# Performance work log

Hardware: AMD Instinct MI355X
Metric: run time of the kernel (lower is better)

Reference implementation:

```python
import jax, jax.numpy as jnp
import numpy as np

B, NV, FD = 16, 128, 8192
T_TEMP = 0.2      # self.T
MARGIN = 1.0      # nn.TripletMarginLoss default
EPS = 1e-6        # pairwise_distance eps


def _l2norm(x):
    # torch F.normalize(dim=1): x / max(||x||, 1e-12)
    nrm = jnp.maximum(jnp.linalg.norm(x, axis=-1, keepdims=True), 1e-12)
    return x / nrm


def _ssl_parts(qb, kb, nb, num_gt):
    # qb,kb,nb: [NV, FD] flattened reid embeddings for one image
    qv = _l2norm(qb)[:num_gt]          # [g, FD]
    kv = _l2norm(kb)[:num_gt]          # [g, FD]
    nv = _l2norm(nb)                   # [NV, FD] (negatives are NOT sliced)
    g = num_gt
    S = qv @ kv.T                      # [g, g] all pairwise dots (replaces torch.dot loops)
    # similarity-matrix loss
    sm = jnp.sum((S - jnp.eye(g, dtype=S.dtype)) ** 2) / (g * g)
    # pairwise distances with torch eps convention: ||a - b + eps||_2
    # = sqrt(||a||^2 + ||b||^2 - 2 a.b + 2*eps*(sum(a)-sum(b)) + D*eps^2); ||a||=||b||=1
    sq = qv.sum(axis=1)                # [g]
    sk = kv.sum(axis=1)                # [g]
    const = FD * EPS * EPS
    d_qk = jnp.sqrt(jnp.maximum(2.0 - 2.0 * S + 2.0 * EPS * (sq[:, None] - sk[None, :]) + const, 0.0))
    d_kq = jnp.sqrt(jnp.maximum(2.0 - 2.0 * S.T + 2.0 * EPS * (sk[:, None] - sq[None, :]) + const, 0.0))
    off = 1.0 - jnp.eye(g, dtype=S.dtype)
    # triplet: anc=q_i,pos=k_i,neg=k_j  and  anc=k_i,pos=q_i,neg=q_j, j != i
    tri1 = jnp.sum(jax.nn.relu(jnp.diag(d_qk)[:, None] - d_qk + MARGIN) * off)
    tri2 = jnp.sum(jax.nn.relu(jnp.diag(d_kq)[:, None] - d_kq + MARGIN) * off)
    tri_sum = tri1 + tri2
    # cycle consistency: |q_i.k_j - k_i.q_j| = |S[i,j] - S[j,i]|
    cyc = jnp.sum(jnp.abs(S - S.T) * off) / (g * (g - 1))
    # InfoNCE: l_pos = q_i.k_i, l_neg = q @ n.T
    l_pos = jnp.diag(S)[:, None]       # [g, 1]
    l_neg = qv @ nv.T                  # [g, NV]
    logits = jnp.concatenate([l_pos, l_neg], axis=1) / T_TEMP
    ce = jnp.mean(jax.nn.logsumexp(logits, axis=1) - logits[:, 0])  # CE with labels=0
    return sm, tri_sum, cyc, ce / g


def setup_inputs() -> dict:
    key = jax.random.key(0)
    kq, kk, kn = jax.random.split(key, 3)
    q = jax.random.normal(kq, (B, NV, FD), dtype=jnp.float32)
    k = jax.random.normal(kk, (B, NV, FD), dtype=jnp.float32)
    n = jax.random.normal(kn, (B, NV, FD), dtype=jnp.float32)
    return {"q": q, "k": k, "n": n, "num_gt": NV}


def reference(q, k, n, num_gt):
    sm, tri, cyc, ce = jax.vmap(lambda a, b, c: _ssl_parts(a, b, c, num_gt))(q, k, n)
    tri_cnt = 2 * num_gt * (num_gt - 1)
    # original bug: tri_loss accumulates across batches while tri_cnt resets,
    # so each batch contributes cumsum(tri)[b] / tri_cnt
    ssl = jnp.sum(sm) + jnp.sum(jnp.cumsum(tri)) / tri_cnt + jnp.sum(cyc) + jnp.sum(ce)
    return ssl
```

## Files before the change

kernel.cpp:

```cpp
#include <hip/hip_runtime.h>
#include <cstdint>
#include <cstddef>

#define B_N   16
#define G_N   128
#define FD_N  8192
#define KSPLIT 16
#define KC    512
#define BK2   32
#define NITER 16

typedef unsigned short u16;
typedef u16  u16x4 __attribute__((ext_vector_type(4)));
typedef u16  u16x8 __attribute__((ext_vector_type(8)));
typedef __bf16 bf16x8 __attribute__((ext_vector_type(8)));
typedef float f32x16 __attribute__((ext_vector_type(16)));

#define QSUM_P   0
#define QSSQ_P   32768
#define KSUM_P   65536
#define KSSQ_P   98304
#define NSSQ_P   131072
#define SM_ROW   163840
#define CE_ROW   165888
#define S_OFF    167936
#define CONTRIB  430080
#define PART_OFF_F 430208

__device__ __forceinline__ u16 f2bf(float f) {
    uint32_t u = __float_as_uint(f);
    u += 0x7FFFu + ((u >> 16) & 1u);
    return (u16)(u >> 16);
}

#define LDS_BARRIER() asm volatile("s_waitcnt lgkmcnt(0)\n\ts_barrier" ::: "memory")

__global__ __launch_bounds__(512, 4)
void k_gemm(const float* __restrict__ q, const float* __restrict__ kM,
            const float* __restrict__ nM, float* __restrict__ ws)
{
    __shared__ __align__(16) u16 sA[G_N * BK2];
    __shared__ __align__(16) u16 sB[G_N * BK2];

    const int tid = threadIdx.x;
    const int blk = blockIdx.x;
    const int b    = blk >> 5;
    const int rem  = blk & 31;
    const int half = rem >> 4;
    const int kch  = rem & 15;

    const int r0 = tid >> 3;
    const int c8 = tid & 7;

    const size_t mat_off = (size_t)b * (G_N * FD_N) + (size_t)kch * KC + (size_t)(c8 * 4);
    const float* Ap = q + mat_off;
    const float* Bp = (half ? nM : kM) + mat_off;

    float4 la[2][2], lb[2][2];
    float aS[2] = {0,0}, aQ[2] = {0,0}, bS[2] = {0,0}, bQ[2] = {0,0};

    #pragma unroll
    for (int st = 0; st < 2; ++st) {
        const float* A2 = Ap + st * BK2;
        const float* B2 = Bp + st * BK2;
        #pragma unroll
        for (int i = 0; i < 2; ++i) {
            la[st][i] = *(const float4*)(A2 + (size_t)(r0 + 64*i) * FD_N);
            lb[st][i] = *(const float4*)(B2 + (size_t)(r0 + 64*i) * FD_N);
        }
    }

    const int lane  = tid & 63;
    const int wv    = tid >> 6;
    const int wm    = wv >> 2;
    const int wn    = wv & 3;
    const int khalf = lane >> 5;
    const int lrow  = lane & 31;
    const int rA0 = wm*64 + lrow;
    const int rB0 = wn*32 + lrow;

    f32x16 acc[2];
    #pragma unroll
    for (int mb = 0; mb < 2; ++mb)
      #pragma unroll
      for (int e = 0; e < 16; ++e) acc[mb][e] = 0.f;

    for (int kb = 0; kb < NITER; ++kb) {
        const int st = kb & 1;
        LDS_BARRIER();
        #pragma unroll
        for (int i = 0; i < 2; ++i) {
            int row = r0 + 64*i;
            int wof = row*BK2 + (((c8>>1) ^ (row&3))<<3) + ((c8&1)<<2);
            float4 v = la[st][i];
            aS[i] += v.x + v.y + v.z + v.w;
            aQ[i] += v.x*v.x + v.y*v.y + v.z*v.z + v.w*v.w;
            u16x4 h; h[0]=f2bf(v.x); h[1]=f2bf(v.y); h[2]=f2bf(v.z); h[3]=f2bf(v.w);
            *(u16x4*)(sA + wof) = h;
            v = lb[st][i];
            bS[i] += v.x + v.y + v.z + v.w;
            bQ[i] += v.x*v.x + v.y*v.y + v.z*v.z + v.w*v.w;
            u16x4 h2; h2[0]=f2bf(v.x); h2[1]=f2bf(v.y); h2[2]=f2bf(v.z); h2[3]=f2bf(v.w);
            *(u16x4*)(sB + wof) = h2;
        }
        LDS_BARRIER();
        if (kb + 2 < NITER) {
            const float* A2 = Ap + (kb+2) * BK2;
            const float* B2 = Bp + (kb+2) * BK2;
            #pragma unroll
            for (int i = 0; i < 2; ++i) {
                la[st][i] = *(const float4*)(A2 + (size_t)(r0 + 64*i) * FD_N);
                lb[st][i] = *(const float4*)(B2 + (size_t)(r0 + 64*i) * FD_N);
            }
        }
        #pragma unroll
        for (int s = 0; s < 2; ++s) {
            int chunk = s*2 + khalf;
            bf16x8 af[2], bfv;
            #pragma unroll
            for (int mb = 0; mb < 2; ++mb) {
                int row = rA0 + mb*32;
                u16x8 raw = *(const u16x8*)(sA + row*BK2 + ((chunk ^ (row&3))<<3));
                af[mb] = __builtin_bit_cast(bf16x8, raw);
            }
            u16x8 rawb = *(const u16x8*)(sB + rB0*BK2 + ((chunk ^ (rB0&3))<<3));
            bfv = __builtin_bit_cast(bf16x8, rawb);
            acc[0] = __builtin_amdgcn_mfma_f32_32x32x16_bf16(af[0], bfv, acc[0], 0, 0, 0);
            acc[1] = __builtin_amdgcn_mfma_f32_32x32x16_bf16(af[1], bfv, acc[1], 0, 0, 0);
        }
    }

    u16* part = (u16*)(ws + PART_OFF_F) + ((size_t)blk << 14);
    #pragma unroll
    for (int mb = 0; mb < 2; ++mb) {
        int col = wn*32 + lrow;
        int rbase = wm*64 + mb*32 + 4*khalf;
        #pragma unroll
        for (int reg = 0; reg < 16; ++reg) {
            int row = rbase + (reg & 3) + 8*(reg >> 2);
            part[row*G_N + col] = f2bf(acc[mb][reg]);
        }
    }

    #pragma unroll
    for (int i = 0; i < 2; ++i) {
        float sa = aS[i], qa = aQ[i], sb = bS[i], qb = bQ[i];
        #pragma unroll
        for (int m = 4; m >= 1; m >>= 1) {
            sa += __shfl_xor(sa, m, 64); qa += __shfl_xor(qa, m, 64);
            sb += __shfl_xor(sb, m, 64); qb += __shfl_xor(qb, m, 64);
        }
        if (c8 == 0) {
            int o = kch*2048 + b*G_N + (r0 + 64*i);
            if (half == 0) {
                ws[QSUM_P + o] = sa; ws[QSSQ_P + o] = qa;
                ws[KSUM_P + o] = sb; ws[KSSQ_P + o] = qb;
            } else {
                ws[NSSQ_P + o] = qb;
            }
        }
    }
}

__global__ __launch_bounds__(256)
void k_red2(float* __restrict__ ws)
{
    const int blk  = blockIdx.x;
    const int b    = blk >> 4;
    const int half = (blk >> 3) & 1;
    const int rg   = blk & 7;
    const int t    = threadIdx.x;
    const int lr   = t >> 4;
    const int i    = rg*16 + lr;
    const int c8   = t & 15;
    __shared__ float nrm[128];
    __shared__ float invq_s[16];

    if (t < 128) {
        float ss = 0.f;
        const float* p = ws + (half ? NSSQ_P : KSSQ_P) + b*G_N + t;
        #pragma unroll
        for (int kc2 = 0; kc2 < KSPLIT; ++kc2) ss += p[kc2*2048];
        nrm[t] = 1.f / fmaxf(sqrtf(ss), 1e-12f);
    } else if (t < 144) {
        float ss = 0.f;
        const float* p = ws + QSSQ_P + b*G_N + rg*16 + (t - 128);
        #pragma unroll
        for (int kc2 = 0; kc2 < KSPLIT; ++kc2) ss += p[kc2*2048];
        invq_s[t-128] = 1.f / fmaxf(sqrtf(ss), 1e-12f);
    }
    __syncthreads();

    const u16* part = (const u16*)(ws + PART_OFF_F);
    float s[8] = {0,0,0,0,0,0,0,0};
    #pragma unroll
    for (int kc2 = 0; kc2 < KSPLIT; ++kc2) {
        size_t idx = ((size_t)(b*32 + half*16 + kc2) << 14) + i*G_N + c8*8;
        u16x8 h = *(const u16x8*)(part + idx);
        #pragma unroll
        for (int e = 0; e < 8; ++e)
            s[e] += __uint_as_float(((uint32_t)h[e]) << 16);
    }
    const float iq = invq_s[lr];
    if (half == 0) {
        float smacc = 0.f;
        float S8[8];
        #pragma unroll
        for (int e = 0; e < 8; ++e) {
            int j = c8*8 + e;
            S8[e] = s[e] * iq * nrm[j];
            float d = S8[e] - (j == i ? 1.f : 0.f);
            smacc += d*d;
        }
        float* Sp = ws + S_OFF + (size_t)b*16384 + i*G_N + c8*8;
        float4 w0 = {S8[0],S8[1],S8[2],S8[3]};
        float4 w1 = {S8[4],S8[5],S8[6],S8[7]};
        *(float4*)Sp = w0; *(float4*)(Sp+4) = w1;
        #pragma unroll
        for (int m = 8; m >= 1; m >>= 1) smacc += __shfl_xor(smacc, m, 64);
        if (c8 == 0) ws[SM_ROW + b*G_N + i] = smacc;
    } else {
        float eacc = 0.f;
        #pragma unroll
        for (int e = 0; e < 8; ++e)
            eacc += __expf(5.f * s[e] * iq * nrm[c8*8+e]);
        #pragma unroll
        for (int m = 8; m >= 1; m >>= 1) eacc += __shfl_xor(eacc, m, 64);
        if (c8 == 0) ws[CE_ROW + b*G_N + i] = eacc;
    }
}

__global__ __launch_bounds__(256)
void k_epi(float* __restrict__ ws)
{
    const int blk = blockIdx.x;
    const int b   = blk >> 3;
    const int i0  = (blk & 7) * 16;
    const int t   = threadIdx.x;
    __shared__ float sqv[128], skv[128], ddq[128], ddk[128];
    __shared__ float rbuf[4];
    const float c0 = (float)FD_N * 1e-6f * 1e-6f;

    const float* S = ws + S_OFF + (size_t)b * 16384;
    if (t < 128) {
        float qs=0, qq=0, ks=0, kq=0;
        #pragma unroll
        for (int kc2 = 0; kc2 < KSPLIT; ++kc2) {
            int o = kc2*2048 + b*G_N + t;
            qs += ws[QSUM_P + o]; qq += ws[QSSQ_P + o];
            ks += ws[KSUM_P + o]; kq += ws[KSSQ_P + o];
        }
        float iq = 1.f/fmaxf(sqrtf(qq),1e-12f);
        float ik = 1.f/fmaxf(sqrtf(kq),1e-12f);
        float sq = qs*iq, sk = ks*ik;
        sqv[t]=sq; skv[t]=sk;
        float Stt = S[t*G_N + t];
        ddq[t] = sqrtf(fmaxf(2.f - 2.f*Stt + 2e-6f*(sq-sk) + c0, 0.f));
        ddk[t] = sqrtf(fmaxf(2.f - 2.f*Stt + 2e-6f*(sk-sq) + c0, 0.f));
    }
    __syncthreads();

    float tri=0.f, cyc=0.f, ce=0.f, sm=0.f;
    #pragma unroll
    for (int p = 0; p < 8; ++p) {
        int idx = p*256 + t;
        int i = i0 + (idx >> 7), j = idx & 127;
        if (i != j) {
            float S_ij = S[i*G_N + j];
            float dqk = sqrtf(fmaxf(2.f - 2.f*S_ij + 2e-6f*(sqv[i]-skv[j]) + c0, 0.f));
            tri += fmaxf(ddq[i] - dqk + 1.f, 0.f);
            float dkq = sqrtf(fmaxf(2.f - 2.f*S_ij + 2e-6f*(skv[j]-sqv[i]) + c0, 0.f));
            tri += fmaxf(ddk[j] - dkq + 1.f, 0.f);
            cyc += fabsf(S_ij - S[j*G_N + i]);
        }
    }
    if (t < 16) {
        int r = i0 + t;
        float lp = 5.f * S[r*G_N + r];
        ce = __logf(ws[CE_ROW + b*G_N + r] + __expf(lp)) - lp;
        sm = ws[SM_ROW + b*G_N + r];
    }
    float contrib = sm * (1.f/16384.f) + cyc * (1.f/16256.f) + ce * (1.f/16384.f)
                  + (float)(B_N - b) * tri * (1.f/32512.f);
    #pragma unroll
    for (int m = 32; m >= 1; m >>= 1) contrib += __shfl_xor(contrib, m, 64);
    if ((t & 63) == 0) rbuf[t >> 6] = contrib;
    __syncthreads();
    if (t == 0) ws[CONTRIB + blk] = rbuf[0] + rbuf[1] + rbuf[2] + rbuf[3];
}

__global__ void k_fin(const float* __restrict__ ws, float* __restrict__ out)
{
    __shared__ float r2[2];
    int t = threadIdx.x;
    float v = ws[CONTRIB + t];
    #pragma unroll
    for (int m = 32; m >= 1; m >>= 1) v += __shfl_xor(v, m, 64);
    if ((t & 63) == 0) r2[t >> 6] = v;
    __syncthreads();
    if (t == 0) out[0] = r2[0] + r2[1];
}

extern "C" void kernel_launch(void* const* d_in, const int* in_sizes, int n_in,
                              void* d_out, int out_size, void* d_ws, size_t ws_size,
                              hipStream_t stream)
{
    const float* q  = (const float*)d_in[0];
    const float* kM = (const float*)d_in[1];
    const float* nM = (const float*)d_in[2];
    float* ws  = (float*)d_ws;
    float* out = (float*)d_out;

    k_gemm<<<B_N * 2 * KSPLIT, 512, 0, stream>>>(q, kM, nM, ws);
    k_red2<<<256, 256, 0, stream>>>(ws);
    k_epi<<<128, 256, 0, stream>>>(ws);
    k_fin<<<1, 128, 0, stream>>>(ws, out);
}
```

Baseline: 268.6 us.

## Unroll GEMM k-loop by two, change LDS swizzle, fold final reduction into atomics

The GEMM main loop is unrolled by two with named register stages, so the double-buffered prefetch registers are indexed statically instead of through a dynamic stage index. The LDS XOR swizzle now uses (row>>1)&3, which changes the bank-conflict pattern of the bf16 writes and MFMA fragment reads. The final k_fin kernel is removed: k_red2 zeroes the output and k_epi blocks atomically add their contributions, saving one launch. The atomics make the summation order nondeterministic, and correctness relies on k_red2 finishing before k_epi on the same stream.

```diff
diff --git a/kernel.cpp b/kernel.cpp
--- a/kernel.cpp
+++ b/kernel.cpp
@@ -24,8 +24,7 @@
 #define SM_ROW   163840
 #define CE_ROW   165888
 #define S_OFF    167936
-#define CONTRIB  430080
-#define PART_OFF_F 430208
+#define PART_OFF_F 430080
 
 __device__ __forceinline__ u16 f2bf(float f) {
     uint32_t u = __float_as_uint(f);
@@ -56,18 +55,20 @@
     const float* Ap = q + mat_off;
     const float* Bp = (half ? nM : kM) + mat_off;
 
-    float4 la[2][2], lb[2][2];
+    float4 a0[2], b0[2], a1[2], b1[2];
     float aS[2] = {0,0}, aQ[2] = {0,0}, bS[2] = {0,0}, bQ[2] = {0,0};
 
     #pragma unroll
-    for (int st = 0; st < 2; ++st) {
-        const float* A2 = Ap + st * BK2;
-        const float* B2 = Bp + st * BK2;
-        #pragma unroll
-        for (int i = 0; i < 2; ++i) {
-            la[st][i] = *(const float4*)(A2 + (size_t)(r0 + 64*i) * FD_N);
-            lb[st][i] = *(const float4*)(B2 + (size_t)(r0 + 64*i) * FD_N);
-        }
+    for (int i = 0; i < 2; ++i) {
+        size_t ro = (size_t)(r0 + 64*i) * FD_N;
+        a0[i] = *(const float4*)(Ap + ro);
+        b0[i] = *(const float4*)(Bp + ro);
+    }
+    #pragma unroll
+    for (int i = 0; i < 2; ++i) {
+        size_t ro = (size_t)(r0 + 64*i) * FD_N + BK2;
+        a1[i] = *(const float4*)(Ap + ro);
+        b1[i] = *(const float4*)(Bp + ro);
     }
 
     const int lane  = tid & 63;
@@ -79,55 +80,77 @@
     const int rA0 = wm*64 + lrow;
     const int rB0 = wn*32 + lrow;
 
+    int wof[2];
+    #pragma unroll
+    for (int i = 0; i < 2; ++i) {
+        int row = r0 + 64*i;
+        wof[i] = row*BK2 + 8*((c8>>1) ^ ((row>>1)&3)) + 4*(c8&1);
+    }
+
     f32x16 acc[2];
     #pragma unroll
     for (int mb = 0; mb < 2; ++mb)
       #pragma unroll
       for (int e = 0; e < 16; ++e) acc[mb][e] = 0.f;
 
-    for (int kb = 0; kb < NITER; ++kb) {
-        const int st = kb & 1;
+#define STORE_STAGE(AR, BR)                                                   \
+    {                                                                         \
+        _Pragma("unroll")                                                     \
+        for (int i = 0; i < 2; ++i) {                                         \
+            float4 v = AR[i];                                                 \
+            aS[i] += v.x + v.y + v.z + v.w;                                   \
+            aQ[i] += v.x*v.x + v.y*v.y + v.z*v.z + v.w*v.w;                   \
+            u16x4 h; h[0]=f2bf(v.x); h[1]=f2bf(v.y); h[2]=f2bf(v.z); h[3]=f2bf(v.w); \
+            *(u16x4*)(sA + wof[i]) = h;                                       \
+            v = BR[i];                                                        \
+            bS[i] += v.x + v.y + v.z + v.w;                                   \
+            bQ[i] += v.x*v.x + v.y*v.y + v.z*v.z + v.w*v.w;                   \
+            u16x4 h2; h2[0]=f2bf(v.x); h2[1]=f2bf(v.y); h2[2]=f2bf(v.z); h2[3]=f2bf(v.w); \
+            *(u16x4*)(sB + wof[i]) = h2;                                      \
+        }                                                                     \
+    }
+
+#define REFILL(AR, BR, KOFF)                                                  \
+    {                                                                         \
+        _Pragma("unroll")                                                     \
+        for (int i = 0; i < 2; ++i) {                                         \
+            size_t ro = (size_t)(r0 + 64*i) * FD_N + (KOFF);                  \
+            AR[i] = *(const float4*)(Ap + ro);                                \
+            BR[i] = *(const float4*)(Bp + ro);                                \
+        }                                                                     \
+    }
+
+#define MFMA_PHASE()                                                          \
+    {                                                                         \
+        _Pragma("unroll")                                                     \
+        for (int s = 0; s < 2; ++s) {                                         \
+            int chunk = s*2 + khalf;                                          \
+            bf16x8 af0, af1, bfv;                                             \
+            { int row = rA0;                                                  \
+              u16x8 raw = *(const u16x8*)(sA + row*BK2 + 8*(chunk ^ ((row>>1)&3))); \
+              af0 = __builtin_bit_cast(bf16x8, raw); }                        \
+            { int row = rA0 + 32;                                             \
+              u16x8 raw = *(const u16x8*)(sA + row*BK2 + 8*(chunk ^ ((row>>1)&3))); \
+              af1 = __builtin_bit_cast(bf16x8, raw); }                        \
+            { int row = rB0;                                                  \
+              u16x8 raw = *(const u16x8*)(sB + row*BK2 + 8*(chunk ^ ((row>>1)&3))); \
+              bfv = __builtin_bit_cast(bf16x8, raw); }                        \
+            acc[0] = __builtin_amdgcn_mfma_f32_32x32x16_bf16(af0, bfv, acc[0], 0, 0, 0); \
+            acc[1] = __builtin_amdgcn_mfma_f32_32x32x16_bf16(af1, bfv, acc[1], 0, 0, 0); \
+        }                                                                     \
+    }
+
+    for (int kb = 0; kb < NITER; kb += 2) {
         LDS_BARRIER();
-        #pragma unroll
-        for (int i = 0; i < 2; ++i) {
-            int row = r0 + 64*i;
-            int wof = row*BK2 + (((c8>>1) ^ (row&3))<<3) + ((c8&1)<<2);
-            float4 v = la[st][i];
-            aS[i] += v.x + v.y + v.z + v.w;
-            aQ[i] += v.x*v.x + v.y*v.y + v.z*v.z + v.w*v.w;
-            u16x4 h; h[0]=f2bf(v.x); h[1]=f2bf(v.y); h[2]=f2bf(v.z); h[3]=f2bf(v.w);
-            *(u16x4*)(sA + wof) = h;
-            v = lb[st][i];
-            bS[i] += v.x + v.y + v.z + v.w;
-            bQ[i] += v.x*v.x + v.y*v.y + v.z*v.z + v.w*v.w;
-            u16x4 h2; h2[0]=f2bf(v.x); h2[1]=f2bf(v.y); h2[2]=f2bf(v.z); h2[3]=f2bf(v.w);
-            *(u16x4*)(sB + wof) = h2;
-        }
+        STORE_STAGE(a0, b0);
         LDS_BARRIER();
-        if (kb + 2 < NITER) {
-            const float* A2 = Ap + (kb+2) * BK2;
-            const float* B2 = Bp + (kb+2) * BK2;
-            #pragma unroll
-            for (int i = 0; i < 2; ++i) {
-                la[st][i] = *(const float4*)(A2 + (size_t)(r0 + 64*i) * FD_N);
-                lb[st][i] = *(const float4*)(B2 + (size_t)(r0 + 64*i) * FD_N);
-            }
-        }
-        #pragma unroll
-        for (int s = 0; s < 2; ++s) {
-            int chunk = s*2 + khalf;
-            bf16x8 af[2], bfv;
-            #pragma unroll
-            for (int mb = 0; mb < 2; ++mb) {
-                int row = rA0 + mb*32;
-                u16x8 raw = *(const u16x8*)(sA + row*BK2 + ((chunk ^ (row&3))<<3));
-                af[mb] = __builtin_bit_cast(bf16x8, raw);
-            }
-            u16x8 rawb = *(const u16x8*)(sB + rB0*BK2 + ((chunk ^ (rB0&3))<<3));
-            bfv = __builtin_bit_cast(bf16x8, rawb);
-            acc[0] = __builtin_amdgcn_mfma_f32_32x32x16_bf16(af[0], bfv, acc[0], 0, 0, 0);
-            acc[1] = __builtin_amdgcn_mfma_f32_32x32x16_bf16(af[1], bfv, acc[1], 0, 0, 0);
-        }
+        if (kb + 2 < NITER) REFILL(a0, b0, (size_t)(kb+2)*BK2);
+        MFMA_PHASE();
+        LDS_BARRIER();
+        STORE_STAGE(a1, b1);
+        LDS_BARRIER();
+        if (kb + 3 < NITER) REFILL(a1, b1, (size_t)(kb+3)*BK2);
+        MFMA_PHASE();
     }
 
     u16* part = (u16*)(ws + PART_OFF_F) + ((size_t)blk << 14);
@@ -163,7 +186,7 @@
 }
 
 __global__ __launch_bounds__(256)
-void k_red2(float* __restrict__ ws)
+void k_red2(float* __restrict__ ws, float* __restrict__ out)
 {
     const int blk  = blockIdx.x;
     const int b    = blk >> 4;
@@ -176,6 +199,8 @@
     __shared__ float nrm[128];
     __shared__ float invq_s[16];
 
+    if (blk == 0 && t == 0) out[0] = 0.f;
+
     if (t < 128) {
         float ss = 0.f;
         const float* p = ws + (half ? NSSQ_P : KSSQ_P) + b*G_N + t;
@@ -231,7 +256,7 @@
 }
 
 __global__ __launch_bounds__(256)
-void k_epi(float* __restrict__ ws)
+void k_epi(float* __restrict__ ws, float* __restrict__ out)
 {
     const int blk = blockIdx.x;
     const int b   = blk >> 3;
@@ -286,19 +311,7 @@
     for (int m = 32; m >= 1; m >>= 1) contrib += __shfl_xor(contrib, m, 64);
     if ((t & 63) == 0) rbuf[t >> 6] = contrib;
     __syncthreads();
-    if (t == 0) ws[CONTRIB + blk] = rbuf[0] + rbuf[1] + rbuf[2] + rbuf[3];
-}
-
-__global__ void k_fin(const float* __restrict__ ws, float* __restrict__ out)
-{
-    __shared__ float r2[2];
-    int t = threadIdx.x;
-    float v = ws[CONTRIB + t];
-    #pragma unroll
-    for (int m = 32; m >= 1; m >>= 1) v += __shfl_xor(v, m, 64);
-    if ((t & 63) == 0) r2[t >> 6] = v;
-    __syncthreads();
-    if (t == 0) out[0] = r2[0] + r2[1];
+    if (t == 0) atomicAdd(out, rbuf[0] + rbuf[1] + rbuf[2] + rbuf[3]);
 }
 
 extern "C" void kernel_launch(void* const* d_in, const int* in_sizes, int n_in,
@@ -312,7 +325,6 @@
     float* out = (float*)d_out;
 
     k_gemm<<<B_N * 2 * KSPLIT, 512, 0, stream>>>(q, kM, nM, ws);
-    k_red2<<<256, 256, 0, stream>>>(ws);
-    k_epi<<<128, 256, 0, stream>>>(ws);
-    k_fin<<<1, 128, 0, stream>>>(ws, out);
-}
+    k_red2<<<256, 256, 0, stream>>>(ws, out);
+    k_epi<<<128, 256, 0, stream>>>(ws, out);
+}
```

Result: faster. 218.6 us (-18.6%).
